# Performance work log

Measured on AMD Instinct MI355X. Metric: run time of the kernel, lower is better.

Reference implementation:

```python
import jax, jax.numpy as jnp
import numpy as np
import math


def setup_inputs() -> dict:
    key = jax.random.key(0)
    ks = jax.random.split(key, 10)
    b, n, d, h = 2, 1024, 1024, 16
    hd = d // h
    std = 0.02
    x = jax.random.normal(ks[0], (b, n, d), jnp.float32)
    Wq = jax.random.normal(ks[1], (d, d), jnp.float32) * std
    Wk = jax.random.normal(ks[2], (d, d), jnp.float32) * std
    Wv = jax.random.normal(ks[3], (d, d), jnp.float32) * std
    Wo = jax.random.normal(ks[4], (d, d), jnp.float32) * std
    Ww1 = jax.random.normal(ks[5], (d, hd), jnp.float32) * std
    Ww2 = jax.random.normal(ks[6], (hd, d), jnp.float32) * std
    Wb = jax.random.normal(ks[7], (d, h), jnp.float32) * std
    Wf = jax.random.normal(ks[8], (d, h), jnp.float32) * std
    # delta initialized so sigmoid(delta) = threshold = 0.99
    delta = jnp.full((h,), math.log(0.99 / (1.0 - 0.99)), jnp.float32)
    return dict(x=x, Wq=Wq, Wk=Wk, Wv=Wv, Wo=Wo, Ww1=Ww1, Ww2=Ww2, Wb=Wb, Wf=Wf, delta=delta)


def reference(x, Wq, Wk, Wv, Wo, Ww1, Ww2, Wb, Wf, delta):
    b, n, d = x.shape
    h = delta.shape[0]
    hd = d // h
    scale = hd ** -0.5
    q = (x @ Wq).reshape(b, n, h, hd)
    k = (x @ Wk).reshape(b, n, h, hd)
    v = (x @ Wv).reshape(b, n, h, hd)
    w = ((x @ Ww1) @ Ww2).reshape(b, n, h, hd)
    # l2-normalize write directions per head
    w = w * jax.lax.rsqrt(jnp.sum(w * w, axis=-1, keepdims=True) + 1e-6)
    beta = 2.0 * jax.nn.sigmoid(x @ Wb)                      # (b,n,h)
    log_f = jax.nn.log_sigmoid((x @ Wf + delta).astype(jnp.float32))  # (b,n,h)
    bt = jnp.transpose(beta, (0, 2, 1))                      # (b,h,n)
    # PaTH attention: logit_{t,j} = q_t^T H_t H_{t-1} ... H_{j+1} k_j, H_s = I - beta_s w_s w_s^T.
    # UT transform: c_{s,j} = w_s . k_j^{(s-1)} satisfies (I + L) C = tril(W K^T, -1)
    # with L_{s,r} = beta_r (w_s . w_r) for r < s.
    A = jnp.einsum('bshd,brhd->bhsr', w, w)                  # w_s . w_r
    L = jnp.tril(A, -1) * bt[:, :, None, :]                  # (b,h,n,n), strictly lower
    Mlow = jnp.tril(jnp.einsum('bshd,bjhd->bhsj', w, k), -1)
    C = jax.scipy.linalg.solve_triangular(L, Mlow, lower=True, unit_diagonal=True)
    # transformed score: S_{t,j} = q_t.k_j - sum_{j<s<=t} beta_s (q_t.w_s) c_{s,j}
    G = jnp.tril(jnp.einsum('bthd,bshd->bhts', q, w) * bt[:, :, None, :])
    S = jnp.einsum('bthd,bjhd->bhtj', q, k) - G @ C          # (b,h,n,n)
    # forgetting-gate decay: add F_t - F_j (cumulative log-sigmoid gates)
    Fc = jnp.cumsum(jnp.transpose(log_f, (0, 2, 1)), axis=-1)  # (b,h,n)
    logits = S * scale + Fc[..., :, None] - Fc[..., None, :]
    mask = jnp.tril(jnp.ones((n, n), bool))
    logits = jnp.where(mask, logits, -jnp.inf)
    P = jax.nn.softmax(logits, axis=-1)
    o = jnp.einsum('bhtj,bjhd->bthd', P, v).reshape(b, n, d)
    return o @ Wo
```

## Files before the change

### kernel.cpp

```cpp
#include <hip/hip_runtime.h>
#include <hip/hip_bf16.h>

#define DEV static __device__ __forceinline__

constexpr float SM_SCALE = 0.125f;

typedef __attribute__((ext_vector_type(8))) short s16x8;
typedef __attribute__((ext_vector_type(8))) unsigned short u16x8;
typedef __attribute__((ext_vector_type(4))) unsigned short u16x4;
typedef __attribute__((ext_vector_type(4))) float f32x4;

DEV float bf2f(unsigned short u) {
  union { unsigned int i; float f; } v; v.i = ((unsigned int)u) << 16; return v.f;
}
DEV unsigned short f2bf(float f) {
  union { float f; unsigned int i; } v; v.f = f;
  unsigned int r = v.i + 0x7fffu + ((v.i >> 16) & 1u);
  return (unsigned short)(r >> 16);
}
DEV void tri_unrank(int r, int& k, int& i) {
  k = (int)((sqrtf(8.f * r + 1.f) - 1.f) * 0.5f);
  while (k * (k + 1) / 2 > r) --k;
  while ((k + 1) * (k + 2) / 2 <= r) ++k;
  i = r - k * (k + 1) / 2;
}
DEV void glds16(const void* g, void* l) {
  __builtin_amdgcn_global_load_lds(
      (const __attribute__((address_space(1))) void*)g,
      (__attribute__((address_space(3))) void*)l, 16, 0, 0);
}

constexpr size_t OFF_XB   = 0;
constexpr size_t OFF_WQT  = 4194304;
constexpr size_t OFF_BL   = 4194304;
constexpr size_t OFF_WKT  = 6291456;
constexpr size_t OFF_WVT  = 8388608;
constexpr size_t OFF_WOT  = 10485760;
constexpr size_t OFF_W1C  = 12582912;
constexpr size_t OFF_W2T  = 12713984;
constexpr size_t OFF_BETA = 12582912;
constexpr size_t OFF_Q16  = 12845056;
constexpr size_t OFF_K16  = 17039360;
constexpr size_t OFF_VT   = 21233664;
constexpr size_t OFF_WN16 = 25427968;
constexpr size_t OFF_WB16 = 29622272;
constexpr size_t OFF_WNF  = 33816576;
constexpr size_t OFF_OB   = 33816576;
constexpr size_t OFF_BFT  = 38010880;
constexpr size_t OFF_FC   = 38273024;
constexpr size_t OFF_L    = 38404096;
constexpr size_t OFF_CT   = 105512960;
constexpr size_t OFF_G    = 172621824;
constexpr size_t OFF_MR   = 239730688;
constexpr size_t OFF_LR   = 239861760;
constexpr size_t OFF_UI   = 239992832;
constexpr size_t OFF_U128 = 244187136;
constexpr size_t OFF_B256 = 252575744;

__global__ __launch_bounds__(256) void prep_all(
    const float* __restrict__ W0, const float* __restrict__ W1,
    const float* __restrict__ W2, const float* __restrict__ W3,
    const float* __restrict__ Ww1, const float* __restrict__ Ww2,
    const float* __restrict__ x, const float* __restrict__ Wb,
    const float* __restrict__ Wf,
    unsigned short* __restrict__ D0, unsigned short* __restrict__ D1,
    unsigned short* __restrict__ D2, unsigned short* __restrict__ D3,
    unsigned short* __restrict__ W1c, unsigned short* __restrict__ W2T,
    unsigned short* __restrict__ xb, unsigned short* __restrict__ BFT) {
  int bidx = blockIdx.x;
  int t = threadIdx.x;
  if (bidx >= 2096) {
    int e0 = ((bidx - 2096) * 256 + t) * 8;
    int j = e0 >> 10, i0 = e0 & 1023;
    u16x8 o;
#pragma unroll
    for (int e = 0; e < 8; ++e) {
      int i = i0 + e;
      float v = 0.f;
      if (j < 16) v = Wb[i * 16 + j];
      else if (j < 32) v = Wf[i * 16 + (j - 16)];
      o[e] = f2bf(v);
    }
    *(u16x8*)(BFT + e0) = o;
    return;
  }
  if (bidx >= 2064) {
    int i = ((bidx - 2064) * 256 + t) * 8;
    float4 a = *(const float4*)(Ww1 + i);
    float4 b = *(const float4*)(Ww1 + i + 4);
    u16x8 o;
    o[0] = f2bf(a.x); o[1] = f2bf(a.y); o[2] = f2bf(a.z); o[3] = f2bf(a.w);
    o[4] = f2bf(b.x); o[5] = f2bf(b.y); o[6] = f2bf(b.z); o[7] = f2bf(b.w);
    *(u16x8*)(W1c + i) = o;
    return;
  }
  if (bidx >= 1040) {
    int i = ((bidx - 1040) * 256 + t) * 8;
    float4 a = *(const float4*)(x + i);
    float4 b = *(const float4*)(x + i + 4);
    u16x8 o;
    o[0] = f2bf(a.x); o[1] = f2bf(a.y); o[2] = f2bf(a.z); o[3] = f2bf(a.w);
    o[4] = f2bf(b.x); o[5] = f2bf(b.y); o[6] = f2bf(b.z); o[7] = f2bf(b.w);
    *(u16x8*)(xb + i) = o;
    return;
  }
  const float* src; unsigned short* dst; int R, C, c0, r0;
  if (bidx >= 1024) {
    src = Ww2; dst = W2T; R = 64; C = 1024;
    c0 = (bidx - 1024) * 64; r0 = 0;
  } else {
    int z = bidx >> 8, xy = bidx & 255;
    src = z == 0 ? W0 : z == 1 ? W1 : z == 2 ? W2 : W3;
    dst = z == 0 ? D0 : z == 1 ? D1 : z == 2 ? D2 : D3;
    R = 1024; C = 1024;
    c0 = (xy & 15) * 64; r0 = (xy >> 4) * 64;
  }
  __shared__ float tile[64 * 65];
#pragma unroll
  for (int i = 0; i < 16; ++i) {
    int lin = t + i * 256; int r = lin >> 6, c = lin & 63;
    tile[r * 65 + c] = src[(size_t)(r0 + r) * C + c0 + c];
  }
  __syncthreads();
#pragma unroll
  for (int i = 0; i < 16; ++i) {
    int lin = t + i * 256; int c = lin >> 6, r = lin & 63;
    dst[(size_t)(c0 + c) * R + r0 + r] = f2bf(tile[r * 65 + c]);
  }
}

__global__ __launch_bounds__(256) void bgfc(const float* __restrict__ BL,
    const float* __restrict__ delta, float* __restrict__ Beta, float* __restrict__ Fc) {
  int bh = blockIdx.x;
  int b = bh >> 4, h = bh & 15;
  int t = threadIdx.x;
  __shared__ float buf[1024];
  __shared__ float tsum[256];
  float dh = delta[h];
#pragma unroll
  for (int i = 0; i < 4; ++i) {
    int n = t + i * 256;
    int row = (b << 10) + n;
    float braw = BL[row * 64 + h];
    Beta[row * 16 + h] = 2.f / (1.f + __expf(-braw));
    float lraw = BL[row * 64 + 16 + h] + dh;
    buf[n] = (lraw >= 0.f) ? -log1pf(__expf(-lraw)) : (lraw - log1pf(__expf(lraw)));
  }
  __syncthreads();
  float loc[4]; float run = 0.f;
#pragma unroll
  for (int i = 0; i < 4; ++i) { run += buf[t * 4 + i]; loc[i] = run; }
  tsum[t] = run;
  __syncthreads();
  for (int off = 1; off < 256; off <<= 1) {
    float add = (t >= off) ? tsum[t - off] : 0.f;
    __syncthreads();
    tsum[t] += add;
    __syncthreads();
  }
  float excl = tsum[t] - run;
#pragma unroll
  for (int i = 0; i < 4; ++i) Fc[bh * 1024 + t * 4 + i] = excl + loc[i];
}

__global__ __launch_bounds__(256) void proj_big(const unsigned short* __restrict__ xb,
    const unsigned short* __restrict__ WqT, const unsigned short* __restrict__ WkT,
    const unsigned short* __restrict__ WvT, const unsigned short* __restrict__ WfT,
    unsigned short* __restrict__ Q16, unsigned short* __restrict__ K16,
    unsigned short* __restrict__ VT, unsigned short* __restrict__ WNF) {
  int idx = blockIdx.x;
  const unsigned short *A, *BT; unsigned short* out; int m0, n0;
  if (idx < 256) {
    int my = idx >> 4, nx = idx & 15;
    m0 = my * 128; A = xb;
    if (nx < 8) { BT = WqT; out = Q16; n0 = nx * 128; }
    else { BT = WkT; out = K16; n0 = (nx - 8) * 128; }
  } else if (idx < 384) {
    int r = idx - 256; int bz = r >> 6; int rem = r & 63;
    m0 = (rem >> 3) * 128; n0 = (rem & 7) * 128;
    A = WvT; BT = xb + ((size_t)bz << 20); out = VT + ((size_t)bz << 20);
  } else {
    int r2 = idx - 384;
    m0 = (r2 >> 3) * 128; n0 = (r2 & 7) * 128;
    A = xb; BT = WfT; out = WNF;
  }
  int t = threadIdx.x;
  int w = t >> 6, l = t & 63;
  int wr = w >> 1, wc = w & 1;
  int fr = l & 15, fq = l >> 4;
  __shared__ unsigned short As[128 * 64];
  __shared__ unsigned short Bs[128 * 64];
  f32x4 acc[4][4];
#pragma unroll
  for (int m = 0; m < 4; ++m)
#pragma unroll
    for (int c = 0; c < 4; ++c) acc[m][c] = (f32x4){0.f, 0.f, 0.f, 0.f};
  for (int k0 = 0; k0 < 1024; k0 += 64) {
    __syncthreads();
#pragma unroll
    for (int i = 0; i < 4; ++i) {
      int cid = t + i * 256;
      int row = cid >> 3, ch = cid & 7;
      int chs = ch ^ (row & 7);
      glds16(A + (size_t)(m0 + row) * 1024 + k0 + chs * 8, (char*)As + cid * 16);
      glds16(BT + (size_t)(n0 + row) * 1024 + k0 + chs * 8, (char*)Bs + cid * 16);
    }
    __syncthreads();
#pragma unroll
    for (int kh = 0; kh < 2; ++kh) {
      s16x8 af[4], bfv[4];
#pragma unroll
      for (int m = 0; m < 4; ++m) {
        int ra = wr * 64 + 16 * m + fr;
        af[m] = *(const s16x8*)((char*)As + (((ra << 7) + (kh << 6) + (fq << 4)) ^ ((ra & 7) << 4)));
      }
#pragma unroll
      for (int c = 0; c < 4; ++c) {
        int rb = wc * 64 + 16 * c + fr;
        bfv[c] = *(const s16x8*)((char*)Bs + (((rb << 7) + (kh << 6) + (fq << 4)) ^ ((rb & 7) << 4)));
      }
#pragma unroll
      for (int m = 0; m < 4; ++m)
#pragma unroll
        for (int c = 0; c < 4; ++c)
          acc[m][c] = __builtin_amdgcn_mfma_f32_16x16x32_bf16(af[m], bfv[c], acc[m][c], 0, 0, 0);
    }
  }
#pragma unroll
  for (int m = 0; m < 4; ++m) {
#pragma unroll
    for (int c = 0; c < 4; ++c) {
      int col = n0 + wc * 64 + 16 * c + fr;
#pragma unroll
      for (int r = 0; r < 4; ++r) {
        int grow = m0 + wr * 64 + 16 * m + fq * 4 + r;
        out[(size_t)grow * 1024 + col] = f2bf(acc[m][c][r]);
      }
    }
  }
}

template<int F32OUT>
__global__ __launch_bounds__(256) void gemm_nt(const unsigned short* __restrict__ A,
    const unsigned short* __restrict__ BT, void* __restrict__ out,
    int M, int N, int K) {
  __shared__ unsigned short As[64 * 64];
  __shared__ unsigned short Bs[64 * 64];
  int m0 = blockIdx.y * 64, n0 = blockIdx.x * 64;
  int t = threadIdx.x;
  int w = t >> 6, l = t & 63, fr = l & 15;
  int koB = (l >> 4) * 16;
  f32x4 acc[4];
#pragma unroll
  for (int c = 0; c < 4; ++c) acc[c] = (f32x4){0.f, 0.f, 0.f, 0.f};
  for (int k0 = 0; k0 < K; k0 += 64) {
    __syncthreads();
#pragma unroll
    for (int i = 0; i < 2; ++i) {
      int cid = t + i * 256;
      int row = cid >> 3, ch = cid & 7;
      int chs = ch ^ (row & 7);
      glds16(A + (size_t)(m0 + row) * K + k0 + chs * 8, (char*)As + cid * 16);
      glds16(BT + (size_t)(n0 + row) * K + k0 + chs * 8, (char*)Bs + cid * 16);
    }
    __syncthreads();
#pragma unroll
    for (int kh = 0; kh < 2; ++kh) {
      int ra = 16 * w + fr;
      s16x8 a = *(const s16x8*)((char*)As + (((ra << 7) + (kh << 6) + koB) ^ ((ra & 7) << 4)));
#pragma unroll
      for (int c = 0; c < 4; ++c) {
        int rb = 16 * c + fr;
        s16x8 bb = *(const s16x8*)((char*)Bs + (((rb << 7) + (kh << 6) + koB) ^ ((rb & 7) << 4)));
        acc[c] = __builtin_amdgcn_mfma_f32_16x16x32_bf16(a, bb, acc[c], 0, 0, 0);
      }
    }
  }
  int rbase = m0 + 16 * w + ((l >> 4) << 2);
#pragma unroll
  for (int c = 0; c < 4; ++c) {
    int col = n0 + 16 * c + fr;
#pragma unroll
    for (int r = 0; r < 4; ++r) {
      if (F32OUT) ((float*)out)[(size_t)(rbase + r) * N + col] = acc[c][r];
      else ((unsigned short*)out)[(size_t)(rbase + r) * N + col] = f2bf(acc[c][r]);
    }
  }
}

__global__ __launch_bounds__(256) void wnorm2(const unsigned short* __restrict__ WNF,
    const float* __restrict__ Beta, unsigned short* __restrict__ WN,
    unsigned short* __restrict__ WB) {
  int row = blockIdx.x;
  int wave = threadIdx.x >> 6, lane = threadIdx.x & 63;
#pragma unroll
  for (int i = 0; i < 4; ++i) {
    int hh = wave * 4 + i;
    size_t idx = ((size_t)row << 10) + hh * 64 + lane;
    float v = bf2f(WNF[idx]);
    float ss = v * v;
#pragma unroll
    for (int off = 1; off < 64; off <<= 1) ss += __shfl_xor(ss, off);
    float wn = v * rsqrtf(ss + 1e-6f);
    WN[idx] = f2bf(wn);
    WB[idx] = f2bf(wn * Beta[row * 16 + hh]);
  }
}

__global__ __launch_bounds__(256) void pairLG(const unsigned short* __restrict__ WN,
    const unsigned short* __restrict__ Q, const unsigned short* __restrict__ WB,
    unsigned short* __restrict__ Lg, unsigned short* __restrict__ Gg) {
  int idx = blockIdx.x;
  int bh = idx & 31, r0r = idx >> 5;
  int tb2, jb2; tri_unrank(r0r, tb2, jb2);
  int b = bh >> 4, h = bh & 15;
  int m0 = tb2 * 128, n0 = jb2 * 128;
  int t = threadIdx.x;
  int w = t >> 6, l = t & 63;
  int wr = w >> 1, wc = w & 1;
  int fr = l & 15, fq = l >> 4;
  __shared__ unsigned short As[128 * 64];
  __shared__ unsigned short Bs[128 * 64];
  const unsigned short* WNb = WN + ((size_t)b << 20) + h * 64;
  const unsigned short* Qb  = Q + ((size_t)b << 20) + h * 64;
  const unsigned short* WBb = WB + ((size_t)b << 20) + h * 64;
  size_t base = (size_t)bh << 20;
#pragma unroll
  for (int i = 0; i < 4; ++i) {
    int cid = t + i * 256;
    int row = cid >> 3, ch = cid & 7;
    int chs = ch ^ (row & 7);
    glds16(WNb + ((size_t)(m0 + row) << 10) + chs * 8, (char*)As + cid * 16);
    glds16(WBb + ((size_t)(n0 + row) << 10) + chs * 8, (char*)Bs + cid * 16);
  }
  __syncthreads();
  for (int pass = 0; pass < 2; ++pass) {
    f32x4 acc[4][4];
#pragma unroll
    for (int m = 0; m < 4; ++m)
#pragma unroll
      for (int c = 0; c < 4; ++c) acc[m][c] = (f32x4){0.f, 0.f, 0.f, 0.f};
#pragma unroll
    for (int kh = 0; kh < 2; ++kh) {
      s16x8 af[4], bfv[4];
#pragma unroll
      for (int m = 0; m < 4; ++m) {
        int ra = wr * 64 + 16 * m + fr;
        af[m] = *(const s16x8*)((char*)As + (((ra << 7) + (kh << 6) + (fq << 4)) ^ ((ra & 7) << 4)));
      }
#pragma unroll
      for (int c = 0; c < 4; ++c) {
        int rb = wc * 64 + 16 * c + fr;
        bfv[c] = *(const s16x8*)((char*)Bs + (((rb << 7) + (kh << 6) + (fq << 4)) ^ ((rb & 7) << 4)));
      }
#pragma unroll
      for (int m = 0; m < 4; ++m)
#pragma unroll
        for (int c = 0; c < 4; ++c)
          acc[m][c] = __builtin_amdgcn_mfma_f32_16x16x32_bf16(af[m], bfv[c], acc[m][c], 0, 0, 0);
    }
    unsigned short* dst = pass ? Gg : Lg;
#pragma unroll
    for (int m = 0; m < 4; ++m) {
#pragma unroll
      for (int c = 0; c < 4; ++c) {
        int gj = n0 + wc * 64 + 16 * c + fr;
#pragma unroll
        for (int r = 0; r < 4; ++r) {
          int gi = m0 + wr * 64 + 16 * m + fq * 4 + r;
          bool keep = pass ? (gj <= gi) : (gj < gi);
          dst[base + ((size_t)gi << 10) + gj] = f2bf(keep ? -acc[m][c][r] : 0.f);
        }
      }
    }
    if (pass == 0) {
      __syncthreads();
#pragma unroll
      for (int i = 0; i < 4; ++i) {
        int cid = t + i * 256;
        int row = cid >> 3, ch = cid & 7;
        int chs = ch ^ (row & 7);
        glds16(Qb + ((size_t)(m0 + row) << 10) + chs * 8, (char*)As + cid * 16);
      }
      __syncthreads();
    }
  }
}

__global__ __launch_bounds__(256) void score128s(const unsigned short* __restrict__ Q,
    const unsigned short* __restrict__ Kk, const unsigned short* __restrict__ G,
    const unsigned short* __restrict__ CT, unsigned short* __restrict__ Sg) {
  int idx = blockIdx.x;
  int bh = idx & 31, r0r = idx >> 5;
  int k, i; tri_unrank(r0r, k, i);
  int tb2 = (7 - k) + i, jb2 = i;
  int b = bh >> 4, h = bh & 15;
  int m0 = tb2 * 128, n0 = jb2 * 128;
  int t = threadIdx.x;
  int w = t >> 6, l = t & 63;
  int wr = w >> 1, wc = w & 1;
  int fr = l & 15, fq = l >> 4;
  __shared__ unsigned short As[128 * 64];
  __shared__ unsigned short Bs[128 * 64];
  size_t base = (size_t)bh << 20;
  const unsigned short* Qb_ = Q + ((size_t)b << 20) + h * 64;
  const unsigned short* Kb_ = Kk + ((size_t)b << 20) + h * 64;
  const unsigned short* Gb_ = G + base;
  const unsigned short* Cb_ = CT + base;
  int kbase = jb2 * 128;
  int nsteps = 1 + (tb2 - jb2 + 1) * 2;
  f32x4 acc[4][4];
#pragma unroll
  for (int m = 0; m < 4; ++m)
#pragma unroll
    for (int c = 0; c < 4; ++c) acc[m][c] = (f32x4){0.f, 0.f, 0.f, 0.f};
  for (int step = 0; step < nsteps; ++step) {
    const unsigned short* pa; const unsigned short* pb; int koff;
    if (step == 0) { pa = Qb_; pb = Kb_; koff = 0; }
    else { pa = Gb_; pb = Cb_; koff = kbase + (step - 1) * 64; }
    __syncthreads();
#pragma unroll
    for (int i2 = 0; i2 < 4; ++i2) {
      int cid = t + i2 * 256;
      int row = cid >> 3, ch = cid & 7;
      int chs = ch ^ (row & 7);
      glds16(pa + ((size_t)(m0 + row) << 10) + koff + chs * 8, (char*)As + cid * 16);
      glds16(pb + ((size_t)(n0 + row) << 10) + koff + chs * 8, (char*)Bs + cid * 16);
    }
    __syncthreads();
#pragma unroll
    for (int kh = 0; kh < 2; ++kh) {
      s16x8 af[4], bfv[4];
#pragma unroll
      for (int m = 0; m < 4; ++m) {
        int ra = wr * 64 + 16 * m + fr;
        af[m] = *(const s16x8*)((char*)As + (((ra << 7) + (kh << 6) + (fq << 4)) ^ ((ra & 7) << 4)));
      }
#pragma unroll
      for (int c = 0; c < 4; ++c) {
        int rb = wc * 64 + 16 * c + fr;
        bfv[c] = *(const s16x8*)((char*)Bs + (((rb << 7) + (kh << 6) + (fq << 4)) ^ ((rb & 7) << 4)));
      }
#pragma unroll
      for (int m = 0; m < 4; ++m)
#pragma unroll
        for (int c = 0; c < 4; ++c)
          acc[m][c] = __builtin_amdgcn_mfma_f32_16x16x32_bf16(af[m], bfv[c], acc[m][c], 0, 0, 0);
    }
  }
#pragma unroll
  for (int m = 0; m < 4; ++m) {
#pragma unroll
    for (int c = 0; c < 4; ++c) {
      int gj = n0 + wc * 64 + 16 * c + fr;
#pragma unroll
      for (int r = 0; r < 4; ++r) {
        int gi = m0 + wr * 64 + 16 * m + fq * 4 + r;
        Sg[base + ((size_t)gi << 10) + gj] = f2bf(acc[m][c][r]);
      }
    }
  }
}

__global__ __launch_bounds__(256) void inv64(const unsigned short* __restrict__ Lb,
    unsigned short* __restrict__ UI) {
  int ib = blockIdx.x, bh = blockIdx.y;
  int t = threadIdx.x;
  int s0 = ib * 64;
  size_t base = (size_t)bh << 20;
  __shared__ float LD[64 * 65];
  __shared__ unsigned short us[64 * 66];
#pragma unroll
  for (int i = 0; i < 16; ++i) {
    int lin = t + i * 256; int s = lin >> 6, r = lin & 63;
    LD[s * 65 + r] = -bf2f(Lb[base + ((size_t)(s0 + s) << 10) + s0 + r]);
  }
  __syncthreads();
  if (t < 64) {
    float cc[64];
#pragma unroll
    for (int s = 0; s < 64; ++s) cc[s] = (s == t) ? 1.f : 0.f;
#pragma unroll
    for (int r = 0; r < 63; ++r) {
      float val = cc[r];
#pragma unroll
      for (int s = r + 1; s < 64; ++s) cc[s] -= LD[s * 65 + r] * val;
    }
#pragma unroll
    for (int s = 0; s < 64; ++s) us[s * 66 + t] = f2bf(cc[s]);
  }
  __syncthreads();
  size_t ubase = ((size_t)(bh * 16 + ib)) << 12;
#pragma unroll
  for (int i = 0; i < 16; ++i) {
    int lin = t + i * 256; int s = lin >> 6, j = lin & 63;
    UI[ubase + s * 64 + j] = us[s * 66 + j];
  }
}

__global__ __launch_bounds__(256) void u128build(const unsigned short* __restrict__ Lb,
    const unsigned short* __restrict__ UI, unsigned short* __restrict__ U128) {
  int ib = blockIdx.x, bh = blockIdx.y;
  int t = threadIdx.x, w = t >> 6, l = t & 63, fr = l & 15, fq = l >> 4;
  int s0 = ib * 128;
  size_t base = (size_t)bh << 20;
  const unsigned short* Ua = UI + (((size_t)(bh * 16 + 2 * ib)) << 12);
  const unsigned short* Uc = UI + (((size_t)(bh * 16 + 2 * ib + 1)) << 12);
  unsigned short* Uo = U128 + (((size_t)(bh * 8 + ib)) << 14);
  __shared__ unsigned short UaT[64 * 64];
  __shared__ unsigned short T1T[64 * 64];
#pragma unroll
  for (int i = 0; i < 2; ++i) {
    int cid = t + i * 256;
    int s = cid >> 3, ch = cid & 7;
    u16x8 v = *(const u16x8*)(Ua + s * 64 + ch * 8);
#pragma unroll
    for (int e = 0; e < 8; ++e) {
      int j = ch * 8 + e;
      int byt = ((j << 7) + (s << 1)) ^ ((j & 7) << 4);
      *(unsigned short*)((char*)UaT + byt) = v[e];
    }
  }
#pragma unroll
  for (int i = 0; i < 8; ++i) {
    int cid = t + i * 256;
    int row = cid >> 4, ch = cid & 15;
    if (row < 64) {
      if (ch < 8) *(u16x8*)(Uo + row * 128 + ch * 8) = *(const u16x8*)(Ua + row * 64 + ch * 8);
      else { u16x8 z = {0,0,0,0,0,0,0,0}; *(u16x8*)(Uo + row * 128 + ch * 8) = z; }
    } else if (ch >= 8) {
      *(u16x8*)(Uo + row * 128 + ch * 8) = *(const u16x8*)(Uc + (row - 64) * 64 + (ch - 8) * 8);
    }
  }
  __syncthreads();
  f32x4 a1[4];
#pragma unroll
  for (int c = 0; c < 4; ++c) a1[c] = (f32x4){0.f, 0.f, 0.f, 0.f};
#pragma unroll
  for (int kc = 0; kc < 2; ++kc) {
    s16x8 af = *(const s16x8*)(Lb + base + ((size_t)(s0 + 64 + 16 * w + fr) << 10) + s0 + kc * 32 + fq * 8);
#pragma unroll
    for (int c = 0; c < 4; ++c) {
      int j = 16 * c + fr;
      s16x8 bb = *(const s16x8*)((char*)UaT + (((j << 7) + (kc << 6) + (fq << 4)) ^ ((j & 7) << 4)));
      a1[c] = __builtin_amdgcn_mfma_f32_16x16x32_bf16(af, bb, a1[c], 0, 0, 0);
    }
  }
#pragma unroll
  for (int c = 0; c < 4; ++c) {
    int gj = 16 * c + fr;
    int sb = 16 * w + fq * 4;
    u16x4 pk;
#pragma unroll
    for (int r = 0; r < 4; ++r) pk[r] = f2bf(a1[c][r]);
    *(u16x4*)((char*)T1T + (((gj << 7) + (sb << 1)) ^ ((gj & 7) << 4))) = pk;
  }
  __syncthreads();
  f32x4 a2[4];
#pragma unroll
  for (int c = 0; c < 4; ++c) a2[c] = (f32x4){0.f, 0.f, 0.f, 0.f};
#pragma unroll
  for (int kc = 0; kc < 2; ++kc) {
    s16x8 af = *(const s16x8*)(Uc + (16 * w + fr) * 64 + kc * 32 + fq * 8);
#pragma unroll
    for (int c = 0; c < 4; ++c) {
      int j = 16 * c + fr;
      s16x8 bb = *(const s16x8*)((char*)T1T + (((j << 7) + (kc << 6) + (fq << 4)) ^ ((j & 7) << 4)));
      a2[c] = __builtin_amdgcn_mfma_f32_16x16x32_bf16(af, bb, a2[c], 0, 0, 0);
    }
  }
#pragma unroll
  for (int c = 0; c < 4; ++c) {
    int gj = 16 * c + fr;
#pragma unroll
    for (int r = 0; r < 4; ++r)
      Uo[(64 + 16 * w + fq * 4 + r) * 128 + gj] = f2bf(a2[c][r]);
  }
}

__global__ __launch_bounds__(256) void u256build(const unsigned short* __restrict__ Lb,
    const unsigned short* __restrict__ U128, unsigned short* __restrict__ B256) {
  int qb = blockIdx.x, bh = blockIdx.y;
  int t = threadIdx.x, w = t >> 6, l = t & 63, fr = l & 15, fq = l >> 4;
  int s0 = qb * 256;
  size_t base = (size_t)bh << 20;
  const unsigned short* Ua = U128 + (((size_t)(bh * 8 + 2 * qb)) << 14);
  const unsigned short* Uc = U128 + (((size_t)(bh * 8 + 2 * qb + 1)) << 14);
  unsigned short* out = B256 + (((size_t)(bh * 4 + qb)) << 14);
  __shared__ unsigned short UaT[16384];
  __shared__ unsigned short T1T[16384];
#pragma unroll
  for (int i = 0; i < 8; ++i) {
    int cid = t + i * 256;
    int s = cid >> 4, ch = cid & 15;
    u16x8 v = *(const u16x8*)(Ua + s * 128 + ch * 8);
#pragma unroll
    for (int e = 0; e < 8; ++e) {
      int j = ch * 8 + e;
      int byt = ((j << 8) + (s << 1)) ^ ((j & 15) << 4);
      *(unsigned short*)((char*)UaT + byt) = v[e];
    }
  }
  __syncthreads();
  f32x4 a1[2][8];
#pragma unroll
  for (int m = 0; m < 2; ++m)
#pragma unroll
    for (int c = 0; c < 8; ++c) a1[m][c] = (f32x4){0.f, 0.f, 0.f, 0.f};
#pragma unroll
  for (int kc = 0; kc < 4; ++kc) {
    s16x8 af[2];
#pragma unroll
    for (int m = 0; m < 2; ++m)
      af[m] = *(const s16x8*)(Lb + base + ((size_t)(s0 + 128 + 32 * w + 16 * m + fr) << 10) + s0 + kc * 32 + fq * 8);
#pragma unroll
    for (int c = 0; c < 8; ++c) {
      int j = 16 * c + fr;
      s16x8 bb = *(const s16x8*)((char*)UaT + (((j << 8) + (kc << 6) + (fq << 4)) ^ ((j & 15) << 4)));
#pragma unroll
      for (int m = 0; m < 2; ++m)
        a1[m][c] = __builtin_amdgcn_mfma_f32_16x16x32_bf16(af[m], bb, a1[m][c], 0, 0, 0);
    }
  }
#pragma unroll
  for (int m = 0; m < 2; ++m) {
#pragma unroll
    for (int c = 0; c < 8; ++c) {
      int col = 16 * c + fr;
      int row0 = 32 * w + 16 * m + fq * 4;
      u16x4 pk;
#pragma unroll
      for (int r = 0; r < 4; ++r) pk[r] = f2bf(a1[m][c][r]);
      int byt = ((col << 8) + (row0 << 1)) ^ ((col & 15) << 4);
      *(u16x4*)((char*)T1T + byt) = pk;
    }
  }
  __syncthreads();
  f32x4 a2[2][8];
#pragma unroll
  for (int m = 0; m < 2; ++m)
#pragma unroll
    for (int c = 0; c < 8; ++c) a2[m][c] = (f32x4){0.f, 0.f, 0.f, 0.f};
#pragma unroll
  for (int kc = 0; kc < 4; ++kc) {
    s16x8 af[2];
#pragma unroll
    for (int m = 0; m < 2; ++m)
      af[m] = *(const s16x8*)(Uc + (32 * w + 16 * m + fr) * 128 + kc * 32 + fq * 8);
#pragma unroll
    for (int c = 0; c < 8; ++c) {
      int j = 16 * c + fr;
      s16x8 bb = *(const s16x8*)((char*)T1T + (((j << 8) + (kc << 6) + (fq << 4)) ^ ((j & 15) << 4)));
#pragma unroll
      for (int m = 0; m < 2; ++m)
        a2[m][c] = __builtin_amdgcn_mfma_f32_16x16x32_bf16(af[m], bb, a2[m][c], 0, 0, 0);
    }
  }
#pragma unroll
  for (int m = 0; m < 2; ++m) {
#pragma unroll
    for (int c = 0; c < 8; ++c) {
      int col = 16 * c + fr;
#pragma unroll
      for (int r = 0; r < 4; ++r)
        out[(32 * w + 16 * m + fq * 4 + r) * 128 + col] = f2bf(a2[m][c][r]);
    }
  }
}

__global__ __launch_bounds__(256) void solve256(const unsigned short* __restrict__ WN,
    const unsigned short* __restrict__ Kk, const unsigned short* __restrict__ Lb,
    const unsigned short* __restrict__ U128, const unsigned short* __restrict__ B256,
    unsigned short* __restrict__ CT, int ib) {
  int jb = blockIdx.x, bh = blockIdx.y;
  int b = bh >> 4, h = bh & 15;
  int t = threadIdx.x, w = t >> 6, l = t & 63, fr = l & 15, fq = l >> 4;
  int s0 = ib * 256, j0 = jb * 128;
  size_t base = (size_t)bh << 20;
  __shared__ unsigned short sh[32768];
  unsigned short* As = sh;
  unsigned short* Bs = sh + 16384;
  unsigned short* rT = sh;
  const unsigned short* Wb_ = WN + ((size_t)b << 20) + h * 64;
  const unsigned short* Kb_ = Kk + ((size_t)b << 20) + h * 64;

  f32x4 acc[4][8];
#pragma unroll
  for (int m = 0; m < 4; ++m)
#pragma unroll
    for (int c = 0; c < 8; ++c) acc[m][c] = (f32x4){0.f, 0.f, 0.f, 0.f};
  int nst = 1 + 4 * ib - 2 * jb; if (nst < 1) nst = 1;
  for (int st = 0; st < nst; ++st) {
    __syncthreads();
    int rb = 2 * jb + st - 1;
#pragma unroll
    for (int i = 0; i < 8; ++i) {
      int cid = t + i * 256;
      int row = cid >> 3, ch = cid & 7;
      int chs = ch ^ (row & 7);
      const unsigned short* ga = (st == 0)
        ? Wb_ + ((size_t)(s0 + row) << 10) + chs * 8
        : Lb + base + ((size_t)(s0 + row) << 10) + rb * 64 + chs * 8;
      glds16(ga, (char*)As + cid * 16);
    }
#pragma unroll
    for (int i = 0; i < 4; ++i) {
      int cid = t + i * 256;
      int row = cid >> 3, ch = cid & 7;
      int chs = ch ^ (row & 7);
      const unsigned short* gb = (st == 0)
        ? Kb_ + ((size_t)(j0 + row) << 10) + chs * 8
        : CT + base + ((size_t)(j0 + row) << 10) + rb * 64 + chs * 8;
      glds16(gb, (char*)Bs + cid * 16);
    }
    __syncthreads();
#pragma unroll
    for (int kh = 0; kh < 2; ++kh) {
      s16x8 af[4], bfv[8];
#pragma unroll
      for (int m = 0; m < 4; ++m) {
        int ra = 64 * w + 16 * m + fr;
        af[m] = *(const s16x8*)((char*)As + (((ra << 7) + (kh << 6) + (fq << 4)) ^ ((ra & 7) << 4)));
      }
#pragma unroll
      for (int c = 0; c < 8; ++c) {
        int rb2 = 16 * c + fr;
        bfv[c] = *(const s16x8*)((char*)Bs + (((rb2 << 7) + (kh << 6) + (fq << 4)) ^ ((rb2 & 7) << 4)));
      }
#pragma unroll
      for (int m = 0; m < 4; ++m)
#pragma unroll
        for (int c = 0; c < 8; ++c)
          acc[m][c] = __builtin_amdgcn_mfma_f32_16x16x32_bf16(af[m], bfv[c], acc[m][c], 0, 0, 0);
    }
  }
  __syncthreads();
#pragma unroll
  for (int m = 0; m < 4; ++m) {
#pragma unroll
    for (int c = 0; c < 8; ++c) {
      int sl0 = 64 * w + 16 * m + fq * 4;
      int jl = 16 * c + fr;
      u16x4 pk;
#pragma unroll
      for (int r = 0; r < 4; ++r) {
        float v = acc[m][c][r];
        if (j0 + jl >= s0 + sl0 + r) v = 0.f;
        pk[r] = f2bf(v);
      }
      int byt = ((jl << 9) + (sl0 << 1)) ^ ((jl & 15) << 4);
      *(u16x4*)((char*)rT + byt) = pk;
    }
  }
  __syncthreads();
  const unsigned short* Ua = U128 + (((size_t)(bh * 8 + 2 * ib)) << 14);
  const unsigned short* Uc = U128 + (((size_t)(bh * 8 + 2 * ib + 1)) << 14);
  const unsigned short* Bm = B256 + (((size_t)(bh * 4 + ib)) << 14);
#pragma unroll
  for (int m = 0; m < 4; ++m)
#pragma unroll
    for (int c = 0; c < 8; ++c) acc[m][c] = (f32x4){0.f, 0.f, 0.f, 0.f};
  int nkc = (w < 2) ? 4 : 8;
  for (int kc = 0; kc < nkc; ++kc) {
    const unsigned short* src; int arow;
    if (w < 2) { src = Ua; arow = 64 * w; }
    else { src = (kc < 4) ? Bm : Uc; arow = 64 * (w - 2); }
    s16x8 uf[4];
#pragma unroll
    for (int m = 0; m < 4; ++m)
      uf[m] = *(const s16x8*)(src + (arow + 16 * m + fr) * 128 + (kc & 3) * 32 + fq * 8);
#pragma unroll
    for (int c = 0; c < 8; ++c) {
      int jl = 16 * c + fr;
      s16x8 bb = *(const s16x8*)((char*)rT + (((jl << 9) + (kc << 6) + (fq << 4)) ^ ((jl & 15) << 4)));
#pragma unroll
      for (int m = 0; m < 4; ++m)
        acc[m][c] = __builtin_amdgcn_mfma_f32_16x16x32_bf16(uf[m], bb, acc[m][c], 0, 0, 0);
    }
  }
#pragma unroll
  for (int m = 0; m < 4; ++m) {
#pragma unroll
    for (int c = 0; c < 8; ++c) {
      int jl = 16 * c + fr;
      int sb = 64 * w + 16 * m + fq * 4;
      u16x4 pk;
#pragma unroll
      for (int r = 0; r < 4; ++r) pk[r] = f2bf(acc[m][c][r]);
      *(u16x4*)(CT + base + ((size_t)(j0 + jl) << 10) + s0 + sb) = pk;
    }
  }
}

__global__ __launch_bounds__(256) void rowstat(const unsigned short* __restrict__ S,
    const float* __restrict__ Fc, float* __restrict__ MR, float* __restrict__ LR) {
  int bh = blockIdx.y;
  int t = blockIdx.x * 4 + (threadIdx.x >> 6);
  int l = threadIdx.x & 63;
  size_t base = (size_t)bh << 20;
  const unsigned short* srow = S + base + ((size_t)t << 10);
  float vals[16]; float vmax = -1e30f;
#pragma unroll
  for (int i = 0; i < 2; ++i) {
    int c0 = i * 512 + l * 8;
    u16x8 sv = *(const u16x8*)(srow + c0);
    float4 f0 = *(const float4*)(Fc + bh * 1024 + c0);
    float4 f1 = *(const float4*)(Fc + bh * 1024 + c0 + 4);
#pragma unroll
    for (int e = 0; e < 8; ++e) {
      float fc = e < 4 ? ((const float*)&f0)[e] : ((const float*)&f1)[e - 4];
      float v = (c0 + e <= t) ? bf2f(sv[e]) * SM_SCALE - fc : -1e30f;
      vals[i * 8 + e] = v; vmax = fmaxf(vmax, v);
    }
  }
#pragma unroll
  for (int o = 1; o < 64; o <<= 1) vmax = fmaxf(vmax, __shfl_xor(vmax, o));
  float sum = 0.f;
#pragma unroll
  for (int e = 0; e < 16; ++e) sum += __expf(vals[e] - vmax);
#pragma unroll
  for (int o = 1; o < 64; o <<= 1) sum += __shfl_xor(sum, o);
  if (l == 0) { MR[bh * 1024 + t] = vmax; LR[bh * 1024 + t] = sum; }
}

__global__ __launch_bounds__(256) void pv_kernel(const unsigned short* __restrict__ S,
    const unsigned short* __restrict__ VT, const float* __restrict__ Fc,
    const float* __restrict__ MR, const float* __restrict__ LR,
    unsigned short* __restrict__ Ob) {
  int idx = blockIdx.x;
  int bh = idx & 31, rank = idx >> 5;
  int tb = 15 - rank;
  int b = bh >> 4, h = bh & 15;
  int t0 = tb * 64;
  int t = threadIdx.x, w = t >> 6, l = t & 63, fr = l & 15, fq = l >> 4;
  __shared__ unsigned short Pl[64 * 64];
  size_t base = (size_t)bh << 20;
  f32x4 acc[4];
#pragma unroll
  for (int c = 0; c < 4; ++c) acc[c] = (f32x4){0.f,0.f,0.f,0.f};
  for (int jb = 0; jb <= tb; ++jb) {
    int j0 = jb * 64;
    __syncthreads();
#pragma unroll
    for (int i = 0; i < 2; ++i) {
      int cid = t + i * 256;
      int row = cid >> 3, ch = cid & 7;
      int grow = t0 + row;
      u16x8 sv = *(const u16x8*)(S + base + ((size_t)grow << 10) + j0 + ch * 8);
      float4 f0 = *(const float4*)(Fc + bh * 1024 + j0 + ch * 8);
      float4 f1 = *(const float4*)(Fc + bh * 1024 + j0 + ch * 8 + 4);
      float m = MR[bh * 1024 + grow];
      u16x8 pv;
#pragma unroll
      for (int e = 0; e < 8; ++e) {
        float fc = e < 4 ? ((const float*)&f0)[e] : ((const float*)&f1)[e - 4];
        float p = __expf(bf2f(sv[e]) * SM_SCALE - fc - m);
        if (jb == tb && ch * 8 + e > row) p = 0.f;
        pv[e] = f2bf(p);
      }
      int byt = ((row << 7) + (ch << 4)) ^ ((row & 7) << 4);
      *(u16x8*)((char*)Pl + byt) = pv;
    }
    __syncthreads();
#pragma unroll
    for (int kh = 0; kh < 2; ++kh) {
      int ra = 16 * w + fr;
      s16x8 a = *(const s16x8*)((char*)Pl + (((ra << 7) + (kh << 6) + (fq << 4)) ^ ((ra & 7) << 4)));
#pragma unroll
      for (int c = 0; c < 4; ++c) {
        s16x8 bb = *(const s16x8*)(VT + ((size_t)bh * 64 + 16 * c + fr) * 1024 + j0 + kh * 32 + fq * 8);
        acc[c] = __builtin_amdgcn_mfma_f32_16x16x32_bf16(a, bb, acc[c], 0, 0, 0);
      }
    }
  }
  float inv[4];
#pragma unroll
  for (int r = 0; r < 4; ++r) inv[r] = 1.f / LR[bh * 1024 + t0 + 16 * w + fq * 4 + r];
#pragma unroll
  for (int c = 0; c < 4; ++c) {
#pragma unroll
    for (int r = 0; r < 4; ++r) {
      int grow = t0 + 16 * w + fq * 4 + r;
      Ob[((size_t)(b * 1024) + grow) * 1024 + h * 64 + 16 * c + fr] = f2bf(acc[c][r] * inv[r]);
    }
  }
}

extern "C" void kernel_launch(void* const* d_in, const int* in_sizes, int n_in,
                              void* d_out, int out_size, void* d_ws, size_t ws_size,
                              hipStream_t stream) {
  const float* x    = (const float*)d_in[0];
  const float* Wq   = (const float*)d_in[1];
  const float* Wk   = (const float*)d_in[2];
  const float* Wv   = (const float*)d_in[3];
  const float* Wo   = (const float*)d_in[4];
  const float* Ww1  = (const float*)d_in[5];
  const float* Ww2  = (const float*)d_in[6];
  const float* Wb   = (const float*)d_in[7];
  const float* Wf   = (const float*)d_in[8];
  const float* delta= (const float*)d_in[9];

  char* ws = (char*)d_ws;
  unsigned short* xb   = (unsigned short*)(ws + OFF_XB);
  unsigned short* WqT  = (unsigned short*)(ws + OFF_WQT);
  float*          BL   = (float*)(ws + OFF_BL);
  unsigned short* WkT  = (unsigned short*)(ws + OFF_WKT);
  unsigned short* WvT  = (unsigned short*)(ws + OFF_WVT);
  unsigned short* WoT  = (unsigned short*)(ws + OFF_WOT);
  unsigned short* W1c  = (unsigned short*)(ws + OFF_W1C);
  unsigned short* W2T  = (unsigned short*)(ws + OFF_W2T);
  float*          Beta = (float*)(ws + OFF_BETA);
  unsigned short* Q16  = (unsigned short*)(ws + OFF_Q16);
  unsigned short* K16  = (unsigned short*)(ws + OFF_K16);
  unsigned short* VT   = (unsigned short*)(ws + OFF_VT);
  unsigned short* WN16 = (unsigned short*)(ws + OFF_WN16);
  unsigned short* WB16 = (unsigned short*)(ws + OFF_WB16);
  unsigned short* WNF16= (unsigned short*)(ws + OFF_WNF);
  unsigned short* ObB  = (unsigned short*)(ws + OFF_OB);
  unsigned short* BFT  = (unsigned short*)(ws + OFF_BFT);
  float*          Fc   = (float*)(ws + OFF_FC);
  unsigned short* Lbuf = (unsigned short*)(ws + OFF_L);
  unsigned short* Sbuf = (unsigned short*)(ws + OFF_L);
  unsigned short* CT   = (unsigned short*)(ws + OFF_CT);
  unsigned short* Gbuf = (unsigned short*)(ws + OFF_G);
  float*          MR   = (float*)(ws + OFF_MR);
  float*          LR   = (float*)(ws + OFF_LR);
  unsigned short* UI   = (unsigned short*)(ws + OFF_UI);
  unsigned short* U128 = (unsigned short*)(ws + OFF_U128);
  unsigned short* B256 = (unsigned short*)(ws + OFF_B256);

  dim3 blk(256);
  prep_all<<<2128, blk, 0, stream>>>(Wq, Wk, Wv, Wo, Ww1, Ww2, x, Wb, Wf,
                                     WqT, WkT, WvT, WoT, W1c, W2T, xb, BFT);
  gemm_nt<0><<<dim3(16,16), blk, 0, stream>>>(W2T, W1c, WN16, 1024, 1024, 64);
  proj_big<<<512, blk, 0, stream>>>(xb, WqT, WkT, WvT, WN16, Q16, K16, VT, WNF16);
  gemm_nt<1><<<dim3(1,32), blk, 0, stream>>>(xb, BFT, BL, 2048, 64, 1024);
  bgfc<<<32, blk, 0, stream>>>(BL, delta, Beta, Fc);
  wnorm2<<<2048, blk, 0, stream>>>(WNF16, Beta, WN16, WB16);
  pairLG<<<dim3(36 * 32), blk, 0, stream>>>(WN16, Q16, WB16, Lbuf, Gbuf);
  inv64<<<dim3(16,32), blk, 0, stream>>>(Lbuf, UI);
  u128build<<<dim3(8,32), blk, 0, stream>>>(Lbuf, UI, U128);
  u256build<<<dim3(4,32), blk, 0, stream>>>(Lbuf, U128, B256);
  for (int ib = 0; ib < 4; ++ib)
    solve256<<<dim3(2 * ib + 2, 32), blk, 0, stream>>>(WN16, K16, Lbuf, U128, B256, CT, ib);
  score128s<<<dim3(36 * 32), blk, 0, stream>>>(Q16, K16, Gbuf, CT, Sbuf);
  rowstat<<<dim3(256,32), blk, 0, stream>>>(Sbuf, Fc, MR, LR);
  pv_kernel<<<dim3(512), blk, 0, stream>>>(Sbuf, VT, Fc, MR, LR, ObB);
  gemm_nt<1><<<dim3(16,32), blk, 0, stream>>>(ObB, WoT, d_out, 2048, 1024, 1024);
}
```

Measured before the change: 316.1 us.

## Fuse beta/forget projection, 64-block inverse, and online softmax into neighbors

Three kernel fusions remove launches and intermediate buffers. The beta/forget gate projection becomes an extra tile mode in proj_big, with prep_all's grid enlarged to produce a padded BFT. The 64x64 triangular inverses now run inside the 128-block builder instead of a separate inv64 kernel with a UI round trip. The rowstat pass is replaced by an online softmax in pv_kernel, which saves a full read of S but adds per-tile max/rescale syncs and wastes most of the 128-column tile in the gate projection.

```diff
diff --git a/kernel.cpp b/kernel.cpp
--- a/kernel.cpp
+++ b/kernel.cpp
@@ -32,7 +32,6 @@
 
 constexpr size_t OFF_XB   = 0;
 constexpr size_t OFF_WQT  = 4194304;
-constexpr size_t OFF_BL   = 4194304;
 constexpr size_t OFF_WKT  = 6291456;
 constexpr size_t OFF_WVT  = 8388608;
 constexpr size_t OFF_WOT  = 10485760;
@@ -51,9 +50,7 @@
 constexpr size_t OFF_L    = 38404096;
 constexpr size_t OFF_CT   = 105512960;
 constexpr size_t OFF_G    = 172621824;
-constexpr size_t OFF_MR   = 239730688;
-constexpr size_t OFF_LR   = 239861760;
-constexpr size_t OFF_UI   = 239992832;
+constexpr size_t OFF_BL   = 239730688;
 constexpr size_t OFF_U128 = 244187136;
 constexpr size_t OFF_B256 = 252575744;
 
@@ -166,10 +163,13 @@
 __global__ __launch_bounds__(256) void proj_big(const unsigned short* __restrict__ xb,
     const unsigned short* __restrict__ WqT, const unsigned short* __restrict__ WkT,
     const unsigned short* __restrict__ WvT, const unsigned short* __restrict__ WfT,
+    const unsigned short* __restrict__ BFT,
     unsigned short* __restrict__ Q16, unsigned short* __restrict__ K16,
-    unsigned short* __restrict__ VT, unsigned short* __restrict__ WNF) {
+    unsigned short* __restrict__ VT, unsigned short* __restrict__ WNF,
+    float* __restrict__ BL) {
   int idx = blockIdx.x;
-  const unsigned short *A, *BT; unsigned short* out; int m0, n0;
+  const unsigned short *A, *BT; unsigned short* out = nullptr; int m0, n0;
+  int mode = 0;
   if (idx < 256) {
     int my = idx >> 4, nx = idx & 15;
     m0 = my * 128; A = xb;
@@ -179,10 +179,13 @@
     int r = idx - 256; int bz = r >> 6; int rem = r & 63;
     m0 = (rem >> 3) * 128; n0 = (rem & 7) * 128;
     A = WvT; BT = xb + ((size_t)bz << 20); out = VT + ((size_t)bz << 20);
-  } else {
+  } else if (idx < 512) {
     int r2 = idx - 384;
     m0 = (r2 >> 3) * 128; n0 = (r2 & 7) * 128;
     A = xb; BT = WfT; out = WNF;
+  } else {
+    m0 = (idx - 512) * 128; n0 = 0;
+    A = xb; BT = BFT; mode = 1;
   }
   int t = threadIdx.x;
   int w = t >> 6, l = t & 63;
@@ -234,7 +237,8 @@
 #pragma unroll
       for (int r = 0; r < 4; ++r) {
         int grow = m0 + wr * 64 + 16 * m + fq * 4 + r;
-        out[(size_t)grow * 1024 + col] = f2bf(acc[m][c][r]);
+        if (mode == 0) out[(size_t)grow * 1024 + col] = f2bf(acc[m][c][r]);
+        else if (col < 64) BL[(size_t)grow * 64 + col] = acc[m][c][r];
       }
     }
   }
@@ -462,77 +466,67 @@
   }
 }
 
-__global__ __launch_bounds__(256) void inv64(const unsigned short* __restrict__ Lb,
-    unsigned short* __restrict__ UI) {
-  int ib = blockIdx.x, bh = blockIdx.y;
-  int t = threadIdx.x;
-  int s0 = ib * 64;
-  size_t base = (size_t)bh << 20;
-  __shared__ float LD[64 * 65];
-  __shared__ unsigned short us[64 * 66];
-#pragma unroll
-  for (int i = 0; i < 16; ++i) {
-    int lin = t + i * 256; int s = lin >> 6, r = lin & 63;
-    LD[s * 65 + r] = -bf2f(Lb[base + ((size_t)(s0 + s) << 10) + s0 + r]);
-  }
-  __syncthreads();
-  if (t < 64) {
-    float cc[64];
-#pragma unroll
-    for (int s = 0; s < 64; ++s) cc[s] = (s == t) ? 1.f : 0.f;
-#pragma unroll
-    for (int r = 0; r < 63; ++r) {
-      float val = cc[r];
-#pragma unroll
-      for (int s = r + 1; s < 64; ++s) cc[s] -= LD[s * 65 + r] * val;
-    }
-#pragma unroll
-    for (int s = 0; s < 64; ++s) us[s * 66 + t] = f2bf(cc[s]);
-  }
-  __syncthreads();
-  size_t ubase = ((size_t)(bh * 16 + ib)) << 12;
-#pragma unroll
-  for (int i = 0; i < 16; ++i) {
-    int lin = t + i * 256; int s = lin >> 6, j = lin & 63;
-    UI[ubase + s * 64 + j] = us[s * 66 + j];
-  }
-}
-
-__global__ __launch_bounds__(256) void u128build(const unsigned short* __restrict__ Lb,
-    const unsigned short* __restrict__ UI, unsigned short* __restrict__ U128) {
+__global__ __launch_bounds__(256) void invbuild(const unsigned short* __restrict__ Lb,
+    unsigned short* __restrict__ U128) {
   int ib = blockIdx.x, bh = blockIdx.y;
   int t = threadIdx.x, w = t >> 6, l = t & 63, fr = l & 15, fq = l >> 4;
   int s0 = ib * 128;
   size_t base = (size_t)bh << 20;
-  const unsigned short* Ua = UI + (((size_t)(bh * 16 + 2 * ib)) << 12);
-  const unsigned short* Uc = UI + (((size_t)(bh * 16 + 2 * ib + 1)) << 12);
   unsigned short* Uo = U128 + (((size_t)(bh * 8 + ib)) << 14);
+  __shared__ float LD[2][64 * 65];
+  __shared__ unsigned short UaR[64 * 72];
+  __shared__ unsigned short UcR[64 * 72];
   __shared__ unsigned short UaT[64 * 64];
   __shared__ unsigned short T1T[64 * 64];
 #pragma unroll
-  for (int i = 0; i < 2; ++i) {
-    int cid = t + i * 256;
-    int s = cid >> 3, ch = cid & 7;
-    u16x8 v = *(const u16x8*)(Ua + s * 64 + ch * 8);
-#pragma unroll
-    for (int e = 0; e < 8; ++e) {
-      int j = ch * 8 + e;
-      int byt = ((j << 7) + (s << 1)) ^ ((j & 7) << 4);
-      *(unsigned short*)((char*)UaT + byt) = v[e];
-    }
-  }
+  for (int i = 0; i < 32; ++i) {
+    int lin = t + i * 256;
+    int blk = lin >> 12, s = (lin >> 6) & 63, r = lin & 63;
+    LD[blk][s * 65 + r] = -bf2f(Lb[base + ((size_t)(s0 + blk * 64 + s) << 10) + s0 + blk * 64 + r]);
+  }
+  __syncthreads();
+  if (t < 128) {
+    int blk = t >> 6, j = t & 63;
+    const float* ld = LD[blk];
+    float cc[64];
+#pragma unroll
+    for (int s = 0; s < 64; ++s) cc[s] = (s == j) ? 1.f : 0.f;
+#pragma unroll
+    for (int r = 0; r < 63; ++r) {
+      float val = cc[r];
+#pragma unroll
+      for (int s = r + 1; s < 64; ++s) cc[s] -= ld[s * 65 + r] * val;
+    }
+    if (blk == 0) {
+#pragma unroll
+      for (int s = 0; s < 64; ++s) {
+        unsigned short v = f2bf(cc[s]);
+        UaR[s * 72 + j] = v;
+        *(unsigned short*)((char*)UaT + (((j << 7) + (s << 1)) ^ ((j & 7) << 4))) = v;
+      }
+    } else {
+#pragma unroll
+      for (int s = 0; s < 64; ++s) UcR[s * 72 + j] = f2bf(cc[s]);
+    }
+  }
+  __syncthreads();
 #pragma unroll
   for (int i = 0; i < 8; ++i) {
     int cid = t + i * 256;
     int row = cid >> 4, ch = cid & 15;
+    u16x8 v = {0, 0, 0, 0, 0, 0, 0, 0};
     if (row < 64) {
-      if (ch < 8) *(u16x8*)(Uo + row * 128 + ch * 8) = *(const u16x8*)(Ua + row * 64 + ch * 8);
-      else { u16x8 z = {0,0,0,0,0,0,0,0}; *(u16x8*)(Uo + row * 128 + ch * 8) = z; }
+      if (ch < 8) {
+#pragma unroll
+        for (int e = 0; e < 8; ++e) v[e] = UaR[row * 72 + ch * 8 + e];
+      }
+      *(u16x8*)(Uo + row * 128 + ch * 8) = v;
     } else if (ch >= 8) {
-      *(u16x8*)(Uo + row * 128 + ch * 8) = *(const u16x8*)(Uc + (row - 64) * 64 + (ch - 8) * 8);
-    }
-  }
-  __syncthreads();
+#pragma unroll
+      for (int e = 0; e < 8; ++e) v[e] = UcR[(row - 64) * 72 + (ch - 8) * 8 + e];
+      *(u16x8*)(Uo + row * 128 + ch * 8) = v;
+    }
+  }
   f32x4 a1[4];
 #pragma unroll
   for (int c = 0; c < 4; ++c) a1[c] = (f32x4){0.f, 0.f, 0.f, 0.f};
@@ -561,7 +555,7 @@
   for (int c = 0; c < 4; ++c) a2[c] = (f32x4){0.f, 0.f, 0.f, 0.f};
 #pragma unroll
   for (int kc = 0; kc < 2; ++kc) {
-    s16x8 af = *(const s16x8*)(Uc + (16 * w + fr) * 64 + kc * 32 + fq * 8);
+    s16x8 af = *(const s16x8*)(UcR + (16 * w + fr) * 72 + kc * 32 + fq * 8);
 #pragma unroll
     for (int c = 0; c < 4; ++c) {
       int j = 16 * c + fr;
@@ -792,40 +786,8 @@
   }
 }
 
-__global__ __launch_bounds__(256) void rowstat(const unsigned short* __restrict__ S,
-    const float* __restrict__ Fc, float* __restrict__ MR, float* __restrict__ LR) {
-  int bh = blockIdx.y;
-  int t = blockIdx.x * 4 + (threadIdx.x >> 6);
-  int l = threadIdx.x & 63;
-  size_t base = (size_t)bh << 20;
-  const unsigned short* srow = S + base + ((size_t)t << 10);
-  float vals[16]; float vmax = -1e30f;
-#pragma unroll
-  for (int i = 0; i < 2; ++i) {
-    int c0 = i * 512 + l * 8;
-    u16x8 sv = *(const u16x8*)(srow + c0);
-    float4 f0 = *(const float4*)(Fc + bh * 1024 + c0);
-    float4 f1 = *(const float4*)(Fc + bh * 1024 + c0 + 4);
-#pragma unroll
-    for (int e = 0; e < 8; ++e) {
-      float fc = e < 4 ? ((const float*)&f0)[e] : ((const float*)&f1)[e - 4];
-      float v = (c0 + e <= t) ? bf2f(sv[e]) * SM_SCALE - fc : -1e30f;
-      vals[i * 8 + e] = v; vmax = fmaxf(vmax, v);
-    }
-  }
-#pragma unroll
-  for (int o = 1; o < 64; o <<= 1) vmax = fmaxf(vmax, __shfl_xor(vmax, o));
-  float sum = 0.f;
-#pragma unroll
-  for (int e = 0; e < 16; ++e) sum += __expf(vals[e] - vmax);
-#pragma unroll
-  for (int o = 1; o < 64; o <<= 1) sum += __shfl_xor(sum, o);
-  if (l == 0) { MR[bh * 1024 + t] = vmax; LR[bh * 1024 + t] = sum; }
-}
-
 __global__ __launch_bounds__(256) void pv_kernel(const unsigned short* __restrict__ S,
     const unsigned short* __restrict__ VT, const float* __restrict__ Fc,
-    const float* __restrict__ MR, const float* __restrict__ LR,
     unsigned short* __restrict__ Ob) {
   int idx = blockIdx.x;
   int bh = idx & 31, rank = idx >> 5;
@@ -834,6 +796,8 @@
   int t0 = tb * 64;
   int t = threadIdx.x, w = t >> 6, l = t & 63, fr = l & 15, fq = l >> 4;
   __shared__ unsigned short Pl[64 * 64];
+  __shared__ float mrow[64], lrow[64], crow[64];
+  if (t < 64) { mrow[t] = -1e30f; lrow[t] = 0.f; }
   size_t base = (size_t)bh << 20;
   f32x4 acc[4];
 #pragma unroll
@@ -841,6 +805,7 @@
   for (int jb = 0; jb <= tb; ++jb) {
     int j0 = jb * 64;
     __syncthreads();
+    float vals[2][8], tmax[2];
 #pragma unroll
     for (int i = 0; i < 2; ++i) {
       int cid = t + i * 256;
@@ -849,19 +814,63 @@
       u16x8 sv = *(const u16x8*)(S + base + ((size_t)grow << 10) + j0 + ch * 8);
       float4 f0 = *(const float4*)(Fc + bh * 1024 + j0 + ch * 8);
       float4 f1 = *(const float4*)(Fc + bh * 1024 + j0 + ch * 8 + 4);
-      float m = MR[bh * 1024 + grow];
-      u16x8 pv;
+      float tm = -1e30f;
 #pragma unroll
       for (int e = 0; e < 8; ++e) {
         float fc = e < 4 ? ((const float*)&f0)[e] : ((const float*)&f1)[e - 4];
-        float p = __expf(bf2f(sv[e]) * SM_SCALE - fc - m);
-        if (jb == tb && ch * 8 + e > row) p = 0.f;
-        pv[e] = f2bf(p);
+        float v = bf2f(sv[e]) * SM_SCALE - fc;
+        if (jb == tb && ch * 8 + e > row) v = -1e30f;
+        vals[i][e] = v; tm = fmaxf(tm, v);
+      }
+      tm = fmaxf(tm, __shfl_xor(tm, 1));
+      tm = fmaxf(tm, __shfl_xor(tm, 2));
+      tm = fmaxf(tm, __shfl_xor(tm, 4));
+      tmax[i] = tm;
+    }
+    if ((t & 7) == 0) {
+#pragma unroll
+      for (int i = 0; i < 2; ++i) {
+        int row = (t >> 3) + i * 32;
+        float mo = mrow[row];
+        float mn = fmaxf(mo, tmax[i]);
+        float sc = __expf(mo - mn);
+        crow[row] = sc; mrow[row] = mn;
+        lrow[row] *= sc;
+      }
+    }
+    __syncthreads();
+    float ps[2];
+#pragma unroll
+    for (int i = 0; i < 2; ++i) {
+      int cid = t + i * 256;
+      int row = cid >> 3, ch = cid & 7;
+      float mn = mrow[row];
+      u16x8 pv;
+      float psum = 0.f;
+#pragma unroll
+      for (int e = 0; e < 8; ++e) {
+        float p = __expf(vals[i][e] - mn);
+        psum += p; pv[e] = f2bf(p);
       }
       int byt = ((row << 7) + (ch << 4)) ^ ((row & 7) << 4);
       *(u16x8*)((char*)Pl + byt) = pv;
-    }
-    __syncthreads();
+      psum += __shfl_xor(psum, 1);
+      psum += __shfl_xor(psum, 2);
+      psum += __shfl_xor(psum, 4);
+      ps[i] = psum;
+    }
+    if ((t & 7) == 0) {
+      lrow[t >> 3] += ps[0];
+      lrow[(t >> 3) + 32] += ps[1];
+    }
+    __syncthreads();
+    float cr[4];
+#pragma unroll
+    for (int r = 0; r < 4; ++r) cr[r] = crow[16 * w + fq * 4 + r];
+#pragma unroll
+    for (int c = 0; c < 4; ++c)
+#pragma unroll
+      for (int r = 0; r < 4; ++r) acc[c][r] *= cr[r];
 #pragma unroll
     for (int kh = 0; kh < 2; ++kh) {
       int ra = 16 * w + fr;
@@ -873,9 +882,10 @@
       }
     }
   }
+  __syncthreads();
   float inv[4];
 #pragma unroll
-  for (int r = 0; r < 4; ++r) inv[r] = 1.f / LR[bh * 1024 + t0 + 16 * w + fq * 4 + r];
+  for (int r = 0; r < 4; ++r) inv[r] = 1.f / lrow[16 * w + fq * 4 + r];
 #pragma unroll
   for (int c = 0; c < 4; ++c) {
 #pragma unroll
@@ -903,7 +913,6 @@
   char* ws = (char*)d_ws;
   unsigned short* xb   = (unsigned short*)(ws + OFF_XB);
   unsigned short* WqT  = (unsigned short*)(ws + OFF_WQT);
-  float*          BL   = (float*)(ws + OFF_BL);
   unsigned short* WkT  = (unsigned short*)(ws + OFF_WKT);
   unsigned short* WvT  = (unsigned short*)(ws + OFF_WVT);
   unsigned short* WoT  = (unsigned short*)(ws + OFF_WOT);
@@ -923,28 +932,24 @@
   unsigned short* Sbuf = (unsigned short*)(ws + OFF_L);
   unsigned short* CT   = (unsigned short*)(ws + OFF_CT);
   unsigned short* Gbuf = (unsigned short*)(ws + OFF_G);
-  float*          MR   = (float*)(ws + OFF_MR);
-  float*          LR   = (float*)(ws + OFF_LR);
-  unsigned short* UI   = (unsigned short*)(ws + OFF_UI);
+  float*          BL   = (float*)(ws + OFF_BL);
   unsigned short* U128 = (unsigned short*)(ws + OFF_U128);
   unsigned short* B256 = (unsigned short*)(ws + OFF_B256);
 
   dim3 blk(256);
-  prep_all<<<2128, blk, 0, stream>>>(Wq, Wk, Wv, Wo, Ww1, Ww2, x, Wb, Wf,
+  prep_all<<<2160, blk, 0, stream>>>(Wq, Wk, Wv, Wo, Ww1, Ww2, x, Wb, Wf,
                                      WqT, WkT, WvT, WoT, W1c, W2T, xb, BFT);
   gemm_nt<0><<<dim3(16,16), blk, 0, stream>>>(W2T, W1c, WN16, 1024, 1024, 64);
-  proj_big<<<512, blk, 0, stream>>>(xb, WqT, WkT, WvT, WN16, Q16, K16, VT, WNF16);
-  gemm_nt<1><<<dim3(1,32), blk, 0, stream>>>(xb, BFT, BL, 2048, 64, 1024);
+  proj_big<<<528, blk, 0, stream>>>(xb, WqT, WkT, WvT, WN16, BFT,
+                                    Q16, K16, VT, WNF16, BL);
   bgfc<<<32, blk, 0, stream>>>(BL, delta, Beta, Fc);
   wnorm2<<<2048, blk, 0, stream>>>(WNF16, Beta, WN16, WB16);
   pairLG<<<dim3(36 * 32), blk, 0, stream>>>(WN16, Q16, WB16, Lbuf, Gbuf);
-  inv64<<<dim3(16,32), blk, 0, stream>>>(Lbuf, UI);
-  u128build<<<dim3(8,32), blk, 0, stream>>>(Lbuf, UI, U128);
+  invbuild<<<dim3(8,32), blk, 0, stream>>>(Lbuf, U128);
   u256build<<<dim3(4,32), blk, 0, stream>>>(Lbuf, U128, B256);
   for (int ib = 0; ib < 4; ++ib)
     solve256<<<dim3(2 * ib + 2, 32), blk, 0, stream>>>(WN16, K16, Lbuf, U128, B256, CT, ib);
   score128s<<<dim3(36 * 32), blk, 0, stream>>>(Q16, K16, Gbuf, CT, Sbuf);
-  rowstat<<<dim3(256,32), blk, 0, stream>>>(Sbuf, Fc, MR, LR);
-  pv_kernel<<<dim3(512), blk, 0, stream>>>(Sbuf, VT, Fc, MR, LR, ObB);
+  pv_kernel<<<dim3(512), blk, 0, stream>>>(Sbuf, VT, Fc, ObB);
   gemm_nt<1><<<dim3(16,32), blk, 0, stream>>>(ObB, WoT, d_out, 2048, 1024, 1024);
 }
```

Result: faster. 306.6 us (-3.0%).
